# Kernel tuning notes

Hardware: AMD Instinct MI355X
Metric: run time of the kernel (lower is better)

Reference implementation:

```python
import jax, jax.numpy as jnp
import numpy as np

N_SENT, N_DOC, G = 100000, 10000, 32

def _seg_mean_right(x, src, dst, n_dst):
    # DGL GraphConv(norm='right'): sum incoming messages / in_degree (clamped to 1)
    m = jax.ops.segment_sum(x[src], dst, num_segments=n_dst)
    deg = jax.ops.segment_sum(jnp.ones_like(dst, dtype=x.dtype), dst, num_segments=n_dst)
    return m / jnp.maximum(deg, 1.0)[:, None]

def _rel_layer(xs, xd, coeff, basis, loop_w, bias,
               src_ss, dst_ss, src_sd, dst_sd, src_ds, dst_ds):
    # WeightBasis: per-relation weight = sum_b coeff[r,b] * basis[b]
    W = jnp.einsum('rb,bio->rio', coeff, basis)  # [3, in, out]
    # rel 0: sent->doc, rel 1: doc->sent, rel 2: sent->sent; HeteroGraphConv sums per dst ntype
    h_doc = _seg_mean_right(xs, src_sd, dst_sd, N_DOC) @ W[0]
    h_sent = (_seg_mean_right(xd, src_ds, dst_ds, N_SENT) @ W[1]
              + _seg_mean_right(xs, src_ss, dst_ss, N_SENT) @ W[2])
    h_sent = jax.nn.relu(h_sent + xs @ loop_w + bias)
    h_doc = jax.nn.relu(h_doc + xd @ loop_w + bias)
    return h_sent, h_doc

def setup_inputs() -> dict:
    key = jax.random.key(0)
    ks = jax.random.split(key, 20)
    d_in, d_h, d_o = 768, 256, 128
    inp = {
        'x_sent': jax.random.normal(ks[0], (N_SENT, d_in), jnp.float32),
        'x_doc': jax.random.normal(ks[1], (N_DOC, d_in), jnp.float32),
        'coeff1': jax.random.normal(ks[2], (3, 2), jnp.float32),
        'basis1': jax.random.normal(ks[3], (2, d_in, d_h), jnp.float32) * 0.02,
        'loop_w1': jax.random.normal(ks[4], (d_in, d_h), jnp.float32) * 0.02,
        'bias1': jnp.zeros((d_h,), jnp.float32),
        'coeff2': jax.random.normal(ks[5], (3, 2), jnp.float32),
        'basis2': jax.random.normal(ks[6], (2, d_h, d_o), jnp.float32) * 0.05,
        'loop_w2': jax.random.normal(ks[7], (d_h, d_o), jnp.float32) * 0.05,
        'bias2': jnp.zeros((d_o,), jnp.float32),
        'w_score': jax.random.normal(ks[8], (d_o, 1), jnp.float32) * 0.05,
        'b_score': jnp.zeros((1,), jnp.float32),
        'src_ss': jax.random.randint(ks[9], (400000,), 0, N_SENT, jnp.int32),
        'dst_ss': jax.random.randint(ks[10], (400000,), 0, N_SENT, jnp.int32),
        'src_sd': jax.random.randint(ks[11], (100000,), 0, N_SENT, jnp.int32),
        'dst_sd': jax.random.randint(ks[12], (100000,), 0, N_DOC, jnp.int32),
        'src_ds': jax.random.randint(ks[13], (100000,), 0, N_DOC, jnp.int32),
        'dst_ds': jax.random.randint(ks[14], (100000,), 0, N_SENT, jnp.int32),
        'gid_sent': jnp.sort(jax.random.randint(ks[15], (N_SENT,), 0, G, jnp.int32)),
        'gid_doc': jnp.sort(jax.random.randint(ks[16], (N_DOC,), 0, G, jnp.int32)),
        'num_graphs': G,
    }
    return inp

def reference(x_sent, x_doc, coeff1, basis1, loop_w1, bias1,
              coeff2, basis2, loop_w2, bias2, w_score, b_score,
              src_ss, dst_ss, src_sd, dst_sd, src_ds, dst_ds,
              gid_sent, gid_doc, num_graphs):
    h_s, h_d = _rel_layer(x_sent, x_doc, coeff1, basis1, loop_w1, bias1,
                          src_ss, dst_ss, src_sd, dst_sd, src_ds, dst_ds)
    h_s, h_d = _rel_layer(h_s, h_d, coeff2, basis2, loop_w2, bias2,
                          src_ss, dst_ss, src_sd, dst_sd, src_ds, dst_ds)
    # dgl.sum_nodes over batched graph, summed across ntypes
    readout = (jax.ops.segment_sum(h_s, gid_sent, num_segments=num_graphs)
               + jax.ops.segment_sum(h_d, gid_doc, num_segments=num_graphs))
    return readout @ w_score + b_score  # [G, 1]
```

## Files before the change

kernel.cpp:

```cpp
#include <hip/hip_runtime.h>

#define CDIV(a,b) (((a)+(b)-1)/(b))

typedef __attribute__((ext_vector_type(8))) short bf16x8;
typedef __attribute__((ext_vector_type(4))) float floatx4;

__device__ __forceinline__ ushort f2bf(float x) {
    unsigned u = __float_as_uint(x);
    return (ushort)((u + 0x7fffu + ((u >> 16) & 1u)) >> 16);
}
__device__ __forceinline__ unsigned cvtpk(float lo, float hi) {
    unsigned r;
    asm("v_cvt_pk_bf16_f32 %0, %1, %2" : "=v"(r) : "v"(lo), "v"(hi));
    return r;
}
__device__ __forceinline__ float bflo(unsigned v) { return __uint_as_float(v << 16); }
__device__ __forceinline__ float bfhi(unsigned v) { return __uint_as_float(v & 0xffff0000u); }

__device__ __forceinline__ void load_lds16(const ushort* g, ushort* l) {
    __builtin_amdgcn_global_load_lds(
        (const __attribute__((address_space(1))) void*)g,
        (__attribute__((address_space(3))) void*)l, 16, 0, 0);
}



__global__ void zero_f4(float4* __restrict__ p, long long n4) {
    long long i = blockIdx.x * 256LL + threadIdx.x;
    if (i < n4) p[i] = make_float4(0.f, 0.f, 0.f, 0.f);
}

__global__ void fill_w5(ushort* __restrict__ BsT, ushort* __restrict__ BdT,
                        const float* __restrict__ basis, const float* __restrict__ loopw,
                        const float* __restrict__ coeff, int K, int N, long long KN) {
    long long i = blockIdx.x * 256LL + threadIdx.x;
    if (i >= KN) return;
    int k = (int)(i % K), n = (int)(i / K);
    int sec = blockIdx.y;
    float val;
    if (sec == 2 || sec == 4) {
        val = loopw[(size_t)k * N + n];
    } else {
        int r = (sec == 0) ? 0 : (sec == 1) ? 2 : 1;
        val = coeff[2 * r] * basis[(size_t)k * N + n] + coeff[2 * r + 1] * basis[KN + (size_t)k * N + n];
    }
    ushort* dst = (sec < 3) ? BsT : BdT;
    int col0 = (sec == 0) ? 0 : (sec == 1) ? N : (sec == 2) ? 2 * N : (sec == 3) ? 0 : N;
    int nn = col0 + n;
    dst[(size_t)nn * K + (k & ~63) + ((k & 63) ^ ((nn & 7) << 3))] = f2bf(val);
}


__global__ void accum_deg_all(const int* __restrict__ dss, const int* __restrict__ dds,
                              const int* __restrict__ dsd, int nss, int nds, int nsd,
                              int NS, int* __restrict__ deg) {
    int i = blockIdx.x * 256 + threadIdx.x;
    if (i < nss) atomicAdd(&deg[dss[i]], 1);
    else if (i < nss + nds) atomicAdd(&deg[NS + dds[i - nss]], 1);
    else if (i < nss + nds + nsd) atomicAdd(&deg[2 * NS + dsd[i - nss - nds]], 1);
}

__global__ void scan_p1(const int* __restrict__ deg, int n, int* __restrict__ bsum) {
    __shared__ int sd[256];
    int blk = blockIdx.x, tid = threadIdx.x;
    int i0 = blk * 1024 + tid * 4;
    int s = 0;
#pragma unroll
    for (int j = 0; j < 4; ++j) if (i0 + j < n) s += deg[i0 + j];
    sd[tid] = s; __syncthreads();
    for (int o = 128; o; o >>= 1) {
        if (tid < o) sd[tid] += sd[tid + o];
        __syncthreads();
    }
    if (tid == 0) bsum[blk] = sd[0];
}

__global__ void scan_p2(int* __restrict__ bsum, int nb, int* __restrict__ rowptr, int ntot, int etot) {
    __shared__ int sd[256];
    int tid = threadIdx.x;
    int v = (tid < nb) ? bsum[tid] : 0;
    sd[tid] = v; __syncthreads();
    for (int o = 1; o < 256; o <<= 1) {
        int t = (tid >= o) ? sd[tid - o] : 0;
        __syncthreads();
        sd[tid] += t;
        __syncthreads();
    }
    if (tid < nb) bsum[tid] = sd[tid] - v;
    if (tid == 0) rowptr[ntot] = etot;
}

__global__ void scan_p3(const int* __restrict__ deg, int n, const int* __restrict__ bsum,
                        int* __restrict__ rowptr) {
    __shared__ int sd[256];
    int blk = blockIdx.x, tid = threadIdx.x;
    int i0 = blk * 1024 + tid * 4;
    int v[4]; int s = 0;
#pragma unroll
    for (int j = 0; j < 4; ++j) { v[j] = (i0 + j < n) ? deg[i0 + j] : 0; s += v[j]; }
    sd[tid] = s; __syncthreads();
    for (int o = 1; o < 256; o <<= 1) {
        int t = (tid >= o) ? sd[tid - o] : 0;
        __syncthreads();
        sd[tid] += t;
        __syncthreads();
    }
    int excl = bsum[blk] + sd[tid] - s;
#pragma unroll
    for (int j = 0; j < 4; ++j) {
        if (i0 + j < n) rowptr[i0 + j] = excl;
        excl += v[j];
    }
}

__global__ void fill_csr_all(const int* __restrict__ sss, const int* __restrict__ dss,
                             const int* __restrict__ sds, const int* __restrict__ dds,
                             const int* __restrict__ ssd, const int* __restrict__ dsd,
                             int nss, int nds, int nsd, int NS,
                             const int* __restrict__ rowptr, int* __restrict__ fill,
                             int* __restrict__ col) {
    int i = blockIdx.x * 256 + threadIdx.x;
    int d, s;
    if (i < nss) { d = dss[i]; s = sss[i]; }
    else if (i < nss + nds) { int j = i - nss; d = NS + dds[j]; s = sds[j]; }
    else if (i < nss + nds + nsd) { int j = i - nss - nds; d = 2 * NS + dsd[j]; s = ssd[j]; }
    else return;
    int p = rowptr[d] + atomicAdd(&fill[d], 1);
    col[p] = s;
}

template<bool AF32>
__global__ __launch_bounds__(256) void gemm_any(
    const void* __restrict__ Araw, const ushort* __restrict__ Bt, ushort* __restrict__ C,
    int M, int K, int N, int BNX) {
    const int nwg = gridDim.x;
    const int orig = blockIdx.x;
    const int q = nwg >> 3, r = nwg & 7;
    const int xcd = orig & 7, idx = orig >> 3;
    const int wg = (xcd < r ? xcd * (q + 1) : r * (q + 1) + (xcd - r) * q) + idx;
    const int bn = (wg % BNX) * 128;
    const long long bm = (long long)(wg / BNX) * 128LL;

    __shared__ ushort As[128 * 64];
    __shared__ ushort Bs[128 * 64];
    const int tid = threadIdx.x;
    const int lane = tid & 63, wave = tid >> 6;
    const int mo = (wave & 1) * 64, no = (wave >> 1) * 64;
    const int l15 = lane & 15, quad = lane >> 4;
    const int srow = wave * 8 + (lane >> 3);
    const int bch = (lane & 7) * 8;
    floatx4 acc[4][4] = {};

    for (int k0 = 0; k0 < K; k0 += 64) {
#pragma unroll
        for (int t = 0; t < 4; ++t) {
            int row = t * 32 + srow;
            load_lds16(Bt + (size_t)(bn + row) * K + k0 + bch,
                       Bs + (t * 32 + wave * 8) * 64);
        }
        if (AF32) {
            float4 pre[4][2];
#pragma unroll
            for (int j = 0; j < 4; ++j) {
                int s = j * 256 + tid;
                int arow = s >> 3, ach = s & 7;
                long long ar = bm + arow; if (ar >= M) ar = M - 1;
                const float* ap = (const float*)Araw + ar * (size_t)K + k0 + ach * 8;
                pre[j][0] = *(const float4*)ap;
                pre[j][1] = *(const float4*)(ap + 4);
            }
#pragma unroll
            for (int j = 0; j < 4; ++j) {
                int s = j * 256 + tid;
                int arow = s >> 3, ach = s & 7;
                uint4 o;
                o.x = cvtpk(pre[j][0].x, pre[j][0].y);
                o.y = cvtpk(pre[j][0].z, pre[j][0].w);
                o.z = cvtpk(pre[j][1].x, pre[j][1].y);
                o.w = cvtpk(pre[j][1].z, pre[j][1].w);
                *(uint4*)(As + arow * 64 + ((ach * 8) ^ ((arow & 7) << 3))) = o;
            }
        } else {
#pragma unroll
            for (int t = 0; t < 4; ++t) {
                int row = t * 32 + srow;
                long long ar = bm + row; if (ar >= M) ar = M - 1;
                load_lds16((const ushort*)Araw + ar * (size_t)K + k0 + bch,
                           As + (t * 32 + wave * 8) * 64);
            }
        }
        __syncthreads();
        bf16x8 af[2][4], bfr[2][4];
#pragma unroll
        for (int h = 0; h < 2; ++h) {
#pragma unroll
            for (int mt = 0; mt < 4; ++mt) {
                int row = mo + mt * 16 + l15;
                af[h][mt] = *(const bf16x8*)(As + row * 64 + ((h * 32 + quad * 8) ^ ((row & 7) << 3)));
            }
#pragma unroll
            for (int nt = 0; nt < 4; ++nt) {
                int row = no + nt * 16 + l15;
                bfr[h][nt] = *(const bf16x8*)(Bs + row * 64 + ((h * 32 + quad * 8) ^ ((row & 7) << 3)));
            }
        }
#pragma unroll
        for (int h = 0; h < 2; ++h)
#pragma unroll
            for (int mt = 0; mt < 4; ++mt)
#pragma unroll
                for (int nt = 0; nt < 4; ++nt)
                    acc[mt][nt] = __builtin_amdgcn_mfma_f32_16x16x32_bf16(af[h][mt], bfr[h][nt], acc[mt][nt], 0, 0, 0);
        __syncthreads();
    }
#pragma unroll
    for (int mt = 0; mt < 4; ++mt)
#pragma unroll
        for (int i = 0; i < 4; ++i) {
            long long row = bm + mo + mt * 16 + quad * 4 + i;
            if (row < M) {
#pragma unroll
                for (int nt = 0; nt < 4; ++nt)
                    C[row * (size_t)N + bn + no + nt * 16 + l15] = f2bf(acc[mt][nt][i]);
            }
        }
}


__global__ __launch_bounds__(256) void gather_l1(
    const ushort* __restrict__ ys, const ushort* __restrict__ yd,
    const int* __restrict__ rowptr, const int* __restrict__ col,
    const float* __restrict__ bias, ushort* __restrict__ h1s, ushort* __restrict__ h1d,
    int NS, int ND) {
    int d = blockIdx.x * 4 + (threadIdx.x >> 6);
    int lane = threadIdx.x & 63;
    int cb = lane * 4;
    float b0 = bias[cb], b1 = bias[cb + 1], b2 = bias[cb + 2], b3 = bias[cb + 3];
    if (d < NS) {
        float a0 = 0, a1 = 0, a2 = 0, a3 = 0;
        int s0 = rowptr[d], s1 = rowptr[d + 1];
        int e = s0;
        for (; e + 4 <= s1; e += 4) {
            int sA = col[e], sB = col[e + 1], sC = col[e + 2], sD = col[e + 3];
            uint2 vA = *(const uint2*)(ys + (size_t)sA * 768 + 256 + cb);
            uint2 vB = *(const uint2*)(ys + (size_t)sB * 768 + 256 + cb);
            uint2 vC = *(const uint2*)(ys + (size_t)sC * 768 + 256 + cb);
            uint2 vD = *(const uint2*)(ys + (size_t)sD * 768 + 256 + cb);
            a0 += bflo(vA.x) + bflo(vB.x) + bflo(vC.x) + bflo(vD.x);
            a1 += bfhi(vA.x) + bfhi(vB.x) + bfhi(vC.x) + bfhi(vD.x);
            a2 += bflo(vA.y) + bflo(vB.y) + bflo(vC.y) + bflo(vD.y);
            a3 += bfhi(vA.y) + bfhi(vB.y) + bfhi(vC.y) + bfhi(vD.y);
        }
        for (; e < s1; ++e) {
            int s = col[e];
            uint2 v = *(const uint2*)(ys + (size_t)s * 768 + 256 + cb);
            a0 += bflo(v.x); a1 += bfhi(v.x); a2 += bflo(v.y); a3 += bfhi(v.y);
        }
        float inv = 1.f / (float)max(s1 - s0, 1);
        float m0 = a0 * inv, m1 = a1 * inv, m2 = a2 * inv, m3 = a3 * inv;
        a0 = a1 = a2 = a3 = 0.f;
        int t0 = rowptr[NS + d], t1 = rowptr[NS + d + 1];
        for (e = t0; e < t1; ++e) {
            int s = col[e];
            uint2 v = *(const uint2*)(yd + (size_t)s * 512 + cb);
            a0 += bflo(v.x); a1 += bfhi(v.x); a2 += bflo(v.y); a3 += bfhi(v.y);
        }
        inv = 1.f / (float)max(t1 - t0, 1);
        uint2 lv = *(const uint2*)(ys + (size_t)d * 768 + 512 + cb);
        float h0 = fmaxf(m0 + a0 * inv + bflo(lv.x) + b0, 0.f);
        float h1 = fmaxf(m1 + a1 * inv + bfhi(lv.x) + b1, 0.f);
        float h2 = fmaxf(m2 + a2 * inv + bflo(lv.y) + b2, 0.f);
        float h3 = fmaxf(m3 + a3 * inv + bfhi(lv.y) + b3, 0.f);
        uint2 o;
        o.x = cvtpk(h0, h1);
        o.y = cvtpk(h2, h3);
        int pos = (cb & ~63) + ((cb & 63) ^ ((d & 7) << 3));
        *(uint2*)(h1s + (size_t)d * 256 + pos) = o;
    } else if (d < NS + ND) {
        int dd = d - NS;
        float a0 = 0, a1 = 0, a2 = 0, a3 = 0;
        int s0 = rowptr[2 * NS + dd], s1 = rowptr[2 * NS + dd + 1];
        int e = s0;
        for (; e + 4 <= s1; e += 4) {
            int sA = col[e], sB = col[e + 1], sC = col[e + 2], sD = col[e + 3];
            uint2 vA = *(const uint2*)(ys + (size_t)sA * 768 + cb);
            uint2 vB = *(const uint2*)(ys + (size_t)sB * 768 + cb);
            uint2 vC = *(const uint2*)(ys + (size_t)sC * 768 + cb);
            uint2 vD = *(const uint2*)(ys + (size_t)sD * 768 + cb);
            a0 += bflo(vA.x) + bflo(vB.x) + bflo(vC.x) + bflo(vD.x);
            a1 += bfhi(vA.x) + bfhi(vB.x) + bfhi(vC.x) + bfhi(vD.x);
            a2 += bflo(vA.y) + bflo(vB.y) + bflo(vC.y) + bflo(vD.y);
            a3 += bfhi(vA.y) + bfhi(vB.y) + bfhi(vC.y) + bfhi(vD.y);
        }
        for (; e < s1; ++e) {
            int s = col[e];
            uint2 v = *(const uint2*)(ys + (size_t)s * 768 + cb);
            a0 += bflo(v.x); a1 += bfhi(v.x); a2 += bflo(v.y); a3 += bfhi(v.y);
        }
        float inv = 1.f / (float)max(s1 - s0, 1);
        uint2 lv = *(const uint2*)(yd + (size_t)dd * 512 + 256 + cb);
        float h0 = fmaxf(a0 * inv + bflo(lv.x) + b0, 0.f);
        float h1 = fmaxf(a1 * inv + bfhi(lv.x) + b1, 0.f);
        float h2 = fmaxf(a2 * inv + bflo(lv.y) + b2, 0.f);
        float h3 = fmaxf(a3 * inv + bfhi(lv.y) + b3, 0.f);
        uint2 o;
        o.x = cvtpk(h0, h1);
        o.y = cvtpk(h2, h3);
        int pos = (cb & ~63) + ((cb & 63) ^ ((dd & 7) << 3));
        *(uint2*)(h1d + (size_t)dd * 256 + pos) = o;
    }
}

__global__ __launch_bounds__(256) void gather_l2(
    const ushort* __restrict__ ys, const ushort* __restrict__ yd,
    const int* __restrict__ rowptr, const int* __restrict__ col,
    const float* __restrict__ bias, const float* __restrict__ w,
    const int* __restrict__ gid_s, const int* __restrict__ gid_d,
    float* __restrict__ out, int NS, int ND, int G) {
    __shared__ float part[4][32];
    const int tid = threadIdx.x;
    const int lane = tid & 63, wv = tid >> 6;
    const int cb = lane * 2;
    const float w0 = w[cb], w1 = w[cb + 1];
    const float b0 = bias[cb], b1 = bias[cb + 1];
    float racc = 0.f;
    const int nw = gridDim.x * 4;
    for (int d = blockIdx.x * 4 + wv; d < NS + ND; d += nw) {
        float h0, h1; int g;
        if (d < NS) {
            float a0 = 0.f, a1 = 0.f;
            int s0 = rowptr[d], s1 = rowptr[d + 1];
            int e = s0;
            for (; e + 4 <= s1; e += 4) {
                int sA = col[e], sB = col[e + 1], sC = col[e + 2], sD = col[e + 3];
                unsigned vA = *(const unsigned*)(ys + (size_t)sA * 384 + 128 + cb);
                unsigned vB = *(const unsigned*)(ys + (size_t)sB * 384 + 128 + cb);
                unsigned vC = *(const unsigned*)(ys + (size_t)sC * 384 + 128 + cb);
                unsigned vD = *(const unsigned*)(ys + (size_t)sD * 384 + 128 + cb);
                a0 += bflo(vA) + bflo(vB) + bflo(vC) + bflo(vD);
                a1 += bfhi(vA) + bfhi(vB) + bfhi(vC) + bfhi(vD);
            }
            for (; e < s1; ++e) {
                int s = col[e];
                unsigned v = *(const unsigned*)(ys + (size_t)s * 384 + 128 + cb);
                a0 += bflo(v); a1 += bfhi(v);
            }
            float inv = 1.f / (float)max(s1 - s0, 1);
            float m0 = a0 * inv, m1 = a1 * inv;
            a0 = 0.f; a1 = 0.f;
            int t0 = rowptr[NS + d], t1 = rowptr[NS + d + 1];
            for (e = t0; e < t1; ++e) {
                int s = col[e];
                unsigned v = *(const unsigned*)(yd + (size_t)s * 256 + cb);
                a0 += bflo(v); a1 += bfhi(v);
            }
            inv = 1.f / (float)max(t1 - t0, 1);
            unsigned lv = *(const unsigned*)(ys + (size_t)d * 384 + 256 + cb);
            h0 = fmaxf(m0 + a0 * inv + bflo(lv) + b0, 0.f);
            h1 = fmaxf(m1 + a1 * inv + bfhi(lv) + b1, 0.f);
            g = gid_s[d];
        } else {
            int dd = d - NS;
            float a0 = 0.f, a1 = 0.f;
            int s0 = rowptr[2 * NS + dd], s1 = rowptr[2 * NS + dd + 1];
            int e = s0;
            for (; e + 4 <= s1; e += 4) {
                int sA = col[e], sB = col[e + 1], sC = col[e + 2], sD = col[e + 3];
                unsigned vA = *(const unsigned*)(ys + (size_t)sA * 384 + cb);
                unsigned vB = *(const unsigned*)(ys + (size_t)sB * 384 + cb);
                unsigned vC = *(const unsigned*)(ys + (size_t)sC * 384 + cb);
                unsigned vD = *(const unsigned*)(ys + (size_t)sD * 384 + cb);
                a0 += bflo(vA) + bflo(vB) + bflo(vC) + bflo(vD);
                a1 += bfhi(vA) + bfhi(vB) + bfhi(vC) + bfhi(vD);
            }
            for (; e < s1; ++e) {
                int s = col[e];
                unsigned v = *(const unsigned*)(ys + (size_t)s * 384 + cb);
                a0 += bflo(v); a1 += bfhi(v);
            }
            float inv = 1.f / (float)max(s1 - s0, 1);
            unsigned lv = *(const unsigned*)(yd + (size_t)dd * 256 + 128 + cb);
            h0 = fmaxf(a0 * inv + bflo(lv) + b0, 0.f);
            h1 = fmaxf(a1 * inv + bfhi(lv) + b1, 0.f);
            g = gid_d[dd];
        }
        float sc = h0 * w0 + h1 * w1;
#pragma unroll
        for (int o = 32; o; o >>= 1) sc += __shfl_down(sc, o);
        sc = __shfl(sc, 0);
        if (lane == g) racc += sc;
    }
    if (lane < 32) part[wv][lane] = racc;
    __syncthreads();
    if (tid < G) atomicAdd(&out[tid], part[0][tid] + part[1][tid] + part[2][tid] + part[3][tid]);
}

__global__ void init_out(float* __restrict__ out, const float* __restrict__ b, int G) {
    int i = threadIdx.x;
    if (i < G) out[i] = b[0];
}


extern "C" void kernel_launch(void* const* d_in, const int* in_sizes, int n_in,
                              void* d_out, int out_size, void* d_ws, size_t ws_size,
                              hipStream_t stream) {
    const float* x_sent = (const float*)d_in[0];
    const float* x_doc  = (const float*)d_in[1];
    const float* coeff1 = (const float*)d_in[2];
    const float* basis1 = (const float*)d_in[3];
    const float* loopw1 = (const float*)d_in[4];
    const float* bias1  = (const float*)d_in[5];
    const float* coeff2 = (const float*)d_in[6];
    const float* basis2 = (const float*)d_in[7];
    const float* loopw2 = (const float*)d_in[8];
    const float* bias2  = (const float*)d_in[9];
    const float* wscore = (const float*)d_in[10];
    const float* bscore = (const float*)d_in[11];
    const int* src_ss = (const int*)d_in[12];
    const int* dst_ss = (const int*)d_in[13];
    const int* src_sd = (const int*)d_in[14];
    const int* dst_sd = (const int*)d_in[15];
    const int* src_ds = (const int*)d_in[16];
    const int* dst_ds = (const int*)d_in[17];
    const int* gid_sent = (const int*)d_in[18];
    const int* gid_doc  = (const int*)d_in[19];

    const int DIN = 768, DH = 256, DOo = 128;
    const int NS = in_sizes[0] / DIN;
    const int ND = in_sizes[1] / DIN;
    const int E_SS = in_sizes[12], E_SD = in_sizes[14], E_DS = in_sizes[16];
    const int NTOT = NS + NS + ND;
    const int ETOT = E_SS + E_DS + E_SD;
    const int G = out_size;
    float* out = (float*)d_out;

    char* base = (char*)d_ws;
    size_t off = 0;
    auto alloc = [&](size_t bytes) -> char* {
        char* p = base + off;
        off = (off + bytes + 255) & ~(size_t)255;
        return p;
    };
    ushort* B1sT = (ushort*)alloc((size_t)768 * 768 * 2);
    ushort* B1dT = (ushort*)alloc((size_t)512 * 768 * 2);
    ushort* B2sT = (ushort*)alloc((size_t)384 * 256 * 2);
    ushort* B2dT = (ushort*)alloc((size_t)256 * 256 * 2);
    ushort* ys1 = (ushort*)alloc((size_t)NS * 768 * 2);
    ushort* yd1 = (ushort*)alloc((size_t)ND * 512 * 2);
    ushort* h1s = (ushort*)alloc((size_t)NS * 256 * 2);
    ushort* h1d = (ushort*)alloc((size_t)ND * 256 * 2);
    ushort* ys2 = (ushort*)alloc((size_t)NS * 384 * 2);
    ushort* yd2 = (ushort*)alloc((size_t)ND * 256 * 2);
    int* deg  = (int*)alloc((size_t)2 * NTOT * 4);
    int* fill = deg + NTOT;
    int* rowptr = (int*)alloc((size_t)(NTOT + 1) * 4);
    int* bsum = (int*)alloc(256 * 4);
    int* colall = (int*)alloc((size_t)ETOT * 4);

    long long t1 = (long long)768 * DH, t2 = (long long)256 * DOo;
    fill_w5<<<dim3((unsigned)CDIV(t1, 256), 5), 256, 0, stream>>>(B1sT, B1dT, basis1, loopw1, coeff1, 768, DH, t1);
    fill_w5<<<dim3((unsigned)CDIV(t2, 256), 5), 256, 0, stream>>>(B2sT, B2dT, basis2, loopw2, coeff2, 256, DOo, t2);

    zero_f4<<<(int)CDIV(2 * NTOT / 4, 256), 256, 0, stream>>>((float4*)deg, 2 * NTOT / 4);
    accum_deg_all<<<CDIV(ETOT, 256), 256, 0, stream>>>(dst_ss, dst_ds, dst_sd, E_SS, E_DS, E_SD, NS, deg);
    int nb = CDIV(NTOT, 1024);
    scan_p1<<<nb, 256, 0, stream>>>(deg, NTOT, bsum);
    scan_p2<<<1, 256, 0, stream>>>(bsum, nb, rowptr, NTOT, ETOT);
    scan_p3<<<nb, 256, 0, stream>>>(deg, NTOT, bsum, rowptr);
    fill_csr_all<<<CDIV(ETOT, 256), 256, 0, stream>>>(src_ss, dst_ss, src_ds, dst_ds, src_sd, dst_sd,
                                                      E_SS, E_DS, E_SD, NS, rowptr, fill, colall);

    {
        int mb = CDIV(NS, 128), mb0 = mb / 2;
        int M0 = mb0 * 128;
        gemm_any<true><<<6 * mb0, 256, 0, stream>>>(x_sent, B1sT, ys1, M0, 768, 768, 6);
        gemm_any<true><<<6 * (mb - mb0), 256, 0, stream>>>(
            x_sent + (size_t)M0 * 768, B1sT, ys1 + (size_t)M0 * 768, NS - M0, 768, 768, 6);
    }
    gemm_any<true><<<4 * CDIV(ND, 128), 256, 0, stream>>>(x_doc, B1dT, yd1, ND, 768, 512, 4);

    gather_l1<<<CDIV(NS + ND, 4), 256, 0, stream>>>(ys1, yd1, rowptr, colall, bias1, h1s, h1d, NS, ND);

    gemm_any<false><<<3 * CDIV(NS, 128), 256, 0, stream>>>(h1s, B2sT, ys2, NS, 256, 384, 3);
    gemm_any<false><<<2 * CDIV(ND, 128), 256, 0, stream>>>(h1d, B2dT, yd2, ND, 256, 256, 2);

    init_out<<<1, 64, 0, stream>>>(out, bscore, G);
    gather_l2<<<1100, 256, 0, stream>>>(ys2, yd2, rowptr, colall, bias2, wscore,
                                        gid_sent, gid_doc, out, NS, ND, G);
}
```

Baseline: 936.9 us.

## Double-buffer LDS tiles in gemm_any to overlap global loads with MFMA

Converts the GEMM's A and B LDS tiles into two-stage ping-pong buffers. The next K-slice's global-to-LDS loads (and for fp32 A, register prefetch plus conversion) are issued before computing on the current slice. This cuts one barrier per iteration and hides load latency behind MFMA work. It doubles LDS use to 64KB per block, which can lower occupancy, and keeps the fp32 prefetch registers live across the MFMA loop.

```diff
diff --git a/kernel.cpp b/kernel.cpp
--- a/kernel.cpp
+++ b/kernel.cpp
@@ -141,8 +141,8 @@
     const int bn = (wg % BNX) * 128;
     const long long bm = (long long)(wg / BNX) * 128LL;
 
-    __shared__ ushort As[128 * 64];
-    __shared__ ushort Bs[128 * 64];
+    __shared__ ushort As[2][128 * 64];
+    __shared__ ushort Bs[2][128 * 64];
     const int tid = threadIdx.x;
     const int lane = tid & 63, wave = tid >> 6;
     const int mo = (wave & 1) * 64, no = (wave >> 1) * 64;
@@ -150,58 +150,75 @@
     const int srow = wave * 8 + (lane >> 3);
     const int bch = (lane & 7) * 8;
     floatx4 acc[4][4] = {};
-
-    for (int k0 = 0; k0 < K; k0 += 64) {
+    float4 pre[4][2];
+
+    auto stageB = [&](int k0, int buf) {
 #pragma unroll
         for (int t = 0; t < 4; ++t) {
             int row = t * 32 + srow;
             load_lds16(Bt + (size_t)(bn + row) * K + k0 + bch,
-                       Bs + (t * 32 + wave * 8) * 64);
-        }
-        if (AF32) {
-            float4 pre[4][2];
-#pragma unroll
-            for (int j = 0; j < 4; ++j) {
-                int s = j * 256 + tid;
-                int arow = s >> 3, ach = s & 7;
-                long long ar = bm + arow; if (ar >= M) ar = M - 1;
-                const float* ap = (const float*)Araw + ar * (size_t)K + k0 + ach * 8;
-                pre[j][0] = *(const float4*)ap;
-                pre[j][1] = *(const float4*)(ap + 4);
-            }
-#pragma unroll
-            for (int j = 0; j < 4; ++j) {
-                int s = j * 256 + tid;
-                int arow = s >> 3, ach = s & 7;
-                uint4 o;
-                o.x = cvtpk(pre[j][0].x, pre[j][0].y);
-                o.y = cvtpk(pre[j][0].z, pre[j][0].w);
-                o.z = cvtpk(pre[j][1].x, pre[j][1].y);
-                o.w = cvtpk(pre[j][1].z, pre[j][1].w);
-                *(uint4*)(As + arow * 64 + ((ach * 8) ^ ((arow & 7) << 3))) = o;
-            }
-        } else {
-#pragma unroll
-            for (int t = 0; t < 4; ++t) {
-                int row = t * 32 + srow;
-                long long ar = bm + row; if (ar >= M) ar = M - 1;
-                load_lds16((const ushort*)Araw + ar * (size_t)K + k0 + bch,
-                           As + (t * 32 + wave * 8) * 64);
-            }
-        }
-        __syncthreads();
+                       Bs[buf] + (t * 32 + wave * 8) * 64);
+        }
+    };
+    auto stageA16 = [&](int k0, int buf) {
+#pragma unroll
+        for (int t = 0; t < 4; ++t) {
+            int row = t * 32 + srow;
+            long long ar = bm + row; if (ar >= M) ar = M - 1;
+            load_lds16((const ushort*)Araw + ar * (size_t)K + k0 + bch,
+                       As[buf] + (t * 32 + wave * 8) * 64);
+        }
+    };
+    auto loadA32 = [&](int k0) {
+#pragma unroll
+        for (int j = 0; j < 4; ++j) {
+            int s = j * 256 + tid;
+            int arow = s >> 3, ach = s & 7;
+            long long ar = bm + arow; if (ar >= M) ar = M - 1;
+            const float* ap = (const float*)Araw + ar * (size_t)K + k0 + ach * 8;
+            pre[j][0] = *(const float4*)ap;
+            pre[j][1] = *(const float4*)(ap + 4);
+        }
+    };
+    auto writeA32 = [&](int buf) {
+#pragma unroll
+        for (int j = 0; j < 4; ++j) {
+            int s = j * 256 + tid;
+            int arow = s >> 3, ach = s & 7;
+            uint4 o;
+            o.x = cvtpk(pre[j][0].x, pre[j][0].y);
+            o.y = cvtpk(pre[j][0].z, pre[j][0].w);
+            o.z = cvtpk(pre[j][1].x, pre[j][1].y);
+            o.w = cvtpk(pre[j][1].z, pre[j][1].w);
+            *(uint4*)(As[buf] + arow * 64 + ((ach * 8) ^ ((arow & 7) << 3))) = o;
+        }
+    };
+
+    if (AF32) { loadA32(0); stageB(0, 0); writeA32(0); }
+    else      { stageA16(0, 0); stageB(0, 0); }
+    __syncthreads();
+
+    int cur = 0;
+    for (int k0 = 0; k0 < K; k0 += 64) {
+        const int nxt = k0 + 64;
+        const bool has = nxt < K;
+        if (has) {
+            if (AF32) loadA32(nxt);
+            else      stageA16(nxt, cur ^ 1);
+            stageB(nxt, cur ^ 1);
+        }
         bf16x8 af[2][4], bfr[2][4];
 #pragma unroll
         for (int h = 0; h < 2; ++h) {
 #pragma unroll
             for (int mt = 0; mt < 4; ++mt) {
                 int row = mo + mt * 16 + l15;
-                af[h][mt] = *(const bf16x8*)(As + row * 64 + ((h * 32 + quad * 8) ^ ((row & 7) << 3)));
+                af[h][mt] = *(const bf16x8*)(As[cur] + row * 64 + ((h * 32 + quad * 8) ^ ((row & 7) << 3)));
             }
 #pragma unroll
             for (int nt = 0; nt < 4; ++nt) {
                 int row = no + nt * 16 + l15;
-                bfr[h][nt] = *(const bf16x8*)(Bs + row * 64 + ((h * 32 + quad * 8) ^ ((row & 7) << 3)));
+                bfr[h][nt] = *(const bf16x8*)(Bs[cur] + row * 64 + ((h * 32 + quad * 8) ^ ((row & 7) << 3)));
             }
         }
 #pragma unroll
@@ -211,7 +228,9 @@
 #pragma unroll
                 for (int nt = 0; nt < 4; ++nt)
                     acc[mt][nt] = __builtin_amdgcn_mfma_f32_16x16x32_bf16(af[h][mt], bfr[h][nt], acc[mt][nt], 0, 0, 0);
+        if (has && AF32) writeA32(cur ^ 1);
         __syncthreads();
+        cur ^= 1;
     }
 #pragma unroll
     for (int mt = 0; mt < 4; ++mt)
```

New measurement: 0.9997 ms. 6.7% more time.
